# Performance work log

Hardware: AMD Instinct MI355X
Metric: run time of the kernel (lower is better)

Reference implementation:

```python
import jax, jax.numpy as jnp
import numpy as np

B, E, C = 512, 512, 100000
S, M, LAMDA, ALPHA = 30.0, 0.35, 0.01, 0.5  # s, m, lamda from init; ALPHA = args.alpha (center lr)
EPS = 1e-6


def setup_inputs() -> dict:
    key = jax.random.key(0)
    k1, k2, k3, k4 = jax.random.split(key, 4)
    embedding = jax.random.normal(k1, (B, E), dtype=jnp.float32)
    weights = jax.random.normal(k2, (C, E), dtype=jnp.float32)  # kaiming-init classifier weights
    centers = jax.random.normal(k3, (C, E), dtype=jnp.float32)  # class centers buffer
    label = jax.random.randint(k4, (B,), 0, C, dtype=jnp.int64)
    return {"embedding": embedding, "weights": weights, "centers": centers, "label": label}


def reference(embedding, weights, centers, label):
    rows = jnp.arange(B)
    # LMCL (CosFace) logits: cosine similarity via L2-normalized features and weights
    emb_n = embedding / jnp.linalg.norm(embedding, axis=1, keepdims=True)
    w_n = weights / jnp.linalg.norm(weights, axis=1, keepdims=True)
    logits = jnp.einsum('be,ce->bc', emb_n, w_n)            # [B, C]
    # subtract margin m at the target class, then scale by s
    m_logits = S * logits.at[rows, label].add(-M)
    logp = jax.nn.log_softmax(m_logits, axis=1)
    lmcl_loss = -jnp.mean(logp[rows, label])
    # top-1 precision (%)
    prec = jnp.mean((jnp.argmax(m_logits, axis=1) == label).astype(jnp.float32)) * 100.0
    # center loss: MSE between features and their class centers (centers treated as constant)
    centers_batch = centers[label]                           # [B, E] gather
    center_loss = jnp.mean((embedding - centers_batch) ** 2)
    # center update: scatter-subtract mean-normalized diff (replaces the python loop)
    counts = jnp.zeros((C,), dtype=jnp.float32).at[label].add(1.0)
    appear = counts[label]                                   # [B]
    diff = ALPHA * (centers_batch - embedding) / (appear[:, None] + EPS)
    new_centers = centers.at[label].add(-diff)
    total_loss = lmcl_loss + LAMDA * center_loss
    return prec, total_loss, new_centers
```

## Files before the change

### kernel.cpp

```cpp
#include <hip/hip_runtime.h>
#include <cstdint>
#include <cstddef>

#define B_ROWS 512
#define E_DIM  512
#define C_CLS  100000
#define NT     782

#define S_SC    30.0f
#define M_MRG   0.35f
#define LAMBDA_ 0.01f
#define ALPHA_  0.5f
#define EPS_    1e-6f

#define BM 128
#define BN 128
#define BK 64
#define LPAD 8

typedef __attribute__((ext_vector_type(8))) short bf16x8;
typedef __attribute__((ext_vector_type(4))) float f32x4;

static_assert((size_t)NT * BN >= C_CLS, "tile count");

constexpr size_t WS_PSUM  = 0;
constexpr size_t WS_PMAX  = WS_PSUM + (size_t)NT * B_ROWS * 4;
constexpr size_t WS_CLOSS = WS_PMAX + (size_t)NT * B_ROWS * 4;
constexpr size_t WS_EMBN  = WS_CLOSS + 512;
constexpr size_t WS_IEN   = WS_EMBN + (size_t)B_ROWS * E_DIM * 2;
constexpr size_t WS_COSL  = WS_IEN + 2048;
constexpr size_t WS_CNT   = WS_COSL + 2048;
constexpr size_t WS_RSUM  = WS_CNT + 2048;
constexpr size_t WS_RMAX  = WS_RSUM + 2048;
constexpr size_t WS_WBF   = 4 * 1024 * 1024;
constexpr size_t WS_NEED  = WS_WBF + (size_t)C_CLS * E_DIM * 2;

__device__ __forceinline__ unsigned short f2bf(float f) {
    unsigned u = __float_as_uint(f);
    u += 0x7fffu + ((u >> 16) & 1u);
    return (unsigned short)(u >> 16);
}
__device__ __forceinline__ unsigned fkey(float f) {
    unsigned u = __float_as_uint(f);
    return (u & 0x80000000u) ? ~u : (u | 0x80000000u);
}
__device__ __forceinline__ float unkey(unsigned k) {
    unsigned u = (k & 0x80000000u) ? (k ^ 0x80000000u) : ~k;
    return __uint_as_float(u);
}
__device__ __forceinline__ float waveReduceSum(float v) {
#pragma unroll
    for (int d = 1; d < 64; d <<= 1) v += __shfl_xor(v, d, 64);
    return v;
}
__device__ __forceinline__ unsigned waveReduceMax(unsigned v) {
#pragma unroll
    for (int d = 1; d < 64; d <<= 1) { unsigned o = __shfl_xor(v, d, 64); v = o > v ? o : v; }
    return v;
}
__device__ __forceinline__ float blockReduceSum256(float v, float* s4) {
    v = waveReduceSum(v);
    int w = threadIdx.x >> 6;
    if ((threadIdx.x & 63) == 0) s4[w] = v;
    __syncthreads();
    float r = s4[0] + s4[1] + s4[2] + s4[3];
    __syncthreads();
    return r;
}
__device__ __forceinline__ void g2l16(const void* g, void* l) {
    __builtin_amdgcn_global_load_lds(
        (const __attribute__((address_space(1))) unsigned int*)g,
        (__attribute__((address_space(3))) unsigned int*)l, 16, 0, 0);
}


__global__ __launch_bounds__(256) void emb_prep(const float* __restrict__ emb,
                                                unsigned short* __restrict__ embn,
                                                float* __restrict__ ien) {
    __shared__ float s4[4];
    int b = blockIdx.x, t = threadIdx.x;
    float2 v = *(const float2*)(emb + (size_t)b * E_DIM + t * 2);
    float ss = blockReduceSum256(v.x * v.x + v.y * v.y, s4);
    float inv = 1.0f / sqrtf(ss);
    ushort2 o; o.x = f2bf(v.x * inv); o.y = f2bf(v.y * inv);
    *(ushort2*)(embn + (size_t)b * E_DIM + t * 2) = o;
    if (t == 0) ien[b] = inv;
}

__global__ __launch_bounds__(256) void w_prep(const float* __restrict__ W,
                                              unsigned short* __restrict__ wbf) {
    int row = blockIdx.x * 4 + (threadIdx.x >> 6);
    int lane = threadIdx.x & 63;
    const float* src = W + (size_t)row * E_DIM;
    f32x4 a = *(const f32x4*)(src + lane * 4);
    f32x4 b = *(const f32x4*)(src + 256 + lane * 4);
    float ss = a.x*a.x + a.y*a.y + a.z*a.z + a.w*a.w
             + b.x*b.x + b.y*b.y + b.z*b.z + b.w*b.w;
    ss = waveReduceSum(ss);
    float inv = 1.0f / sqrtf(fmaxf(ss, 1e-30f));
    ushort4 o0, o1;
    o0.x = f2bf(a.x*inv); o0.y = f2bf(a.y*inv); o0.z = f2bf(a.z*inv); o0.w = f2bf(a.w*inv);
    o1.x = f2bf(b.x*inv); o1.y = f2bf(b.y*inv); o1.z = f2bf(b.z*inv); o1.w = f2bf(b.w*inv);
    *(ushort4*)(wbf + (size_t)row * E_DIM + lane * 4) = o0;
    *(ushort4*)(wbf + (size_t)row * E_DIM + 256 + lane * 4) = o1;
}

__global__ __launch_bounds__(256) void label_stats(const float* __restrict__ emb,
                                                   const float* __restrict__ W,
                                                   const float* __restrict__ centers,
                                                   const int* __restrict__ label,
                                                   const float* __restrict__ ien,
                                                   float* __restrict__ cosl,
                                                   float* __restrict__ cntf,
                                                   float* __restrict__ closs) {
    __shared__ float s4[4];
    int b = blockIdx.x, t = threadIdx.x;
    int lab = label[b];
    float d = 0.f, wss = 0.f, sq = 0.f;
    for (int c = t; c < E_DIM; c += 256) {
        float e  = emb[(size_t)b * E_DIM + c];
        float w  = W[(size_t)lab * E_DIM + c];
        float ce = centers[(size_t)lab * E_DIM + c];
        d += e * w; wss += w * w;
        float df = e - ce; sq += df * df;
    }
    float cn = ((label[t] == lab) ? 1.f : 0.f) + ((label[t + 256] == lab) ? 1.f : 0.f);
    d   = blockReduceSum256(d, s4);
    wss = blockReduceSum256(wss, s4);
    sq  = blockReduceSum256(sq, s4);
    cn  = blockReduceSum256(cn, s4);
    if (t == 0) {
        cosl[b] = d * ien[b] / sqrtf(wss);
        cntf[b] = cn;
        atomicAdd(closs, sq);
    }
}

__global__ __launch_bounds__(256) void gemm_fast(const unsigned short* __restrict__ embn,
                                                 const unsigned short* __restrict__ wbf,
                                                 const int* __restrict__ label,
                                                 float* __restrict__ psum,
                                                 unsigned* __restrict__ pmax) {
    __shared__ __align__(16) unsigned short sA[BM * BK];
    __shared__ __align__(16) unsigned short sB[BN * BK];
    __shared__ int      sLab[BM];
    __shared__ float    sSum[BM];
    __shared__ unsigned sMax[BM];

    const int tid = threadIdx.x;
    const int n0 = blockIdx.x * BN;
    const int lane = tid & 63, wave = tid >> 6;
    const int wm = wave >> 1, wn = wave & 1;
    const int q = lane >> 4, lm = lane & 15;
    const int lm7 = lm & 7;

    int aOff[4];
    const unsigned short* bP[4];
    unsigned short *aD[4], *bD[4];
#pragma unroll
    for (int j = 0; j < 4; ++j) {
        int G = j * 256 + tid;
        int r = G >> 3, p = G & 7, l = p ^ (r & 7);
        aOff[j] = r * E_DIM + l * 8;
        int rg = n0 + r; if (rg >= C_CLS) rg = 0;
        bP[j] = wbf + (size_t)rg * E_DIM + l * 8;
        aD[j] = &sA[(j * 256 + wave * 64) * 8];
        bD[j] = &sB[(j * 256 + wave * 64) * 8];
    }

    for (int m = 0; m < 4; ++m) {
        if (tid < BM) { sLab[tid] = label[m * BM + tid]; sSum[tid] = 0.f; sMax[tid] = 0u; }
        const unsigned short* aBase = embn + (size_t)m * BM * E_DIM;

        f32x4 acc[4][4];
#pragma unroll
        for (int i = 0; i < 4; ++i)
#pragma unroll
            for (int j = 0; j < 4; ++j) acc[i][j] = (f32x4){0.f, 0.f, 0.f, 0.f};

        for (int k0 = 0; k0 < E_DIM; k0 += BK) {
            __syncthreads();
#pragma unroll
            for (int j = 0; j < 4; ++j) g2l16(aBase + aOff[j] + k0, aD[j]);
#pragma unroll
            for (int j = 0; j < 4; ++j) g2l16(bP[j] + k0, bD[j]);
            __syncthreads();
#pragma unroll
            for (int kk = 0; kk < BK; kk += 32) {
                const int pg = ((kk >> 3) + q) ^ lm7;
                bf16x8 af[4], bfr[4];
#pragma unroll
                for (int i = 0; i < 4; ++i)
                    af[i] = *(const bf16x8*)&sA[(wm * 64 + i * 16 + lm) * BK + pg * 8];
#pragma unroll
                for (int j = 0; j < 4; ++j)
                    bfr[j] = *(const bf16x8*)&sB[(wn * 64 + j * 16 + lm) * BK + pg * 8];
#pragma unroll
                for (int i = 0; i < 4; ++i)
#pragma unroll
                    for (int j = 0; j < 4; ++j)
                        acc[i][j] = __builtin_amdgcn_mfma_f32_16x16x32_bf16(af[i], bfr[j], acc[i][j], 0, 0, 0);
            }
        }

#pragma unroll
        for (int i = 0; i < 4; ++i) {
#pragma unroll
            for (int r = 0; r < 4; ++r) {
                int row_l = wm * 64 + i * 16 + q * 4 + r;
                int lab = sLab[row_l];
                float sum = 0.f, mx = -1e30f;
#pragma unroll
                for (int j = 0; j < 4; ++j) {
                    int col_l = wn * 64 + j * 16 + lm;
                    int col = n0 + col_l;
                    float v = S_SC * acc[i][j][r];
                    if (col < C_CLS && col != lab) {
                        sum += __expf(v - 30.0f);
                        mx = fmaxf(mx, v);
                    }
                }
#pragma unroll
                for (int d = 1; d < 16; d <<= 1) {
                    sum += __shfl_xor(sum, d, 64);
                    mx = fmaxf(mx, __shfl_xor(mx, d, 64));
                }
                if (lm == 0) {
                    atomicAdd(&sSum[row_l], sum);
                    atomicMax(&sMax[row_l], fkey(mx));
                }
            }
        }
        __syncthreads();
        if (tid < BM) {
            psum[(size_t)blockIdx.x * B_ROWS + m * BM + tid] = sSum[tid];
            pmax[(size_t)blockIdx.x * B_ROWS + m * BM + tid] = sMax[tid];
        }
    }
}

__global__ __launch_bounds__(256) void gemm_slow(const unsigned short* __restrict__ embn,
                                                 const float* __restrict__ W,
                                                 const int* __restrict__ label,
                                                 float* __restrict__ psum,
                                                 unsigned* __restrict__ pmax) {
    __shared__ __align__(16) unsigned short sA[BM][BK + LPAD];
    __shared__ __align__(16) unsigned short sB[BN][BK + LPAD];
    __shared__ int      sLab[BM];
    __shared__ float    sSum[BM];
    __shared__ unsigned sMax[BM];
    __shared__ float    sInvN[BN];

    const int tid = threadIdx.x;
    const int m0 = blockIdx.x * BM;
    const int n0 = blockIdx.y * BN;
    if (tid < BM) { sLab[tid] = label[m0 + tid]; sSum[tid] = 0.f; sMax[tid] = 0u; }

    const int lane = tid & 63;
    const int wave = tid >> 6;
    const int wm = wave >> 1, wn = wave & 1;
    const int q = lane >> 4, lm = lane & 15;

    const int arow = tid >> 3, ac8 = tid & 7;
    const int brow = tid >> 4, bc4 = tid & 15;

    f32x4 acc[4][4];
#pragma unroll
    for (int i = 0; i < 4; ++i)
#pragma unroll
        for (int j = 0; j < 4; ++j) acc[i][j] = (f32x4){0.f, 0.f, 0.f, 0.f};

    float rss[8];
#pragma unroll
    for (int j = 0; j < 8; ++j) rss[j] = 0.f;

    const float* wb = W + (size_t)(n0 + brow) * E_DIM + bc4 * 4;

    for (int k0 = 0; k0 < E_DIM; k0 += BK) {
        __syncthreads();
#pragma unroll
        for (int j = 0; j < 4; ++j) {
            int rr = arow + 32 * j;
            uint4 v = *(const uint4*)(embn + (size_t)(m0 + rr) * E_DIM + k0 + ac8 * 8);
            *(uint4*)(&sA[rr][ac8 * 8]) = v;
        }
#pragma unroll
        for (int j = 0; j < 8; ++j) {
            int rr = brow + 16 * j;
            f32x4 v = (f32x4){0.f, 0.f, 0.f, 0.f};
            if (n0 + rr < C_CLS) v = *(const f32x4*)(wb + (size_t)(16 * j) * E_DIM + k0);
            rss[j] += v.x * v.x + v.y * v.y + v.z * v.z + v.w * v.w;
            ushort4 o; o.x = f2bf(v.x); o.y = f2bf(v.y); o.z = f2bf(v.z); o.w = f2bf(v.w);
            *(ushort4*)(&sB[rr][bc4 * 4]) = o;
        }
        __syncthreads();
#pragma unroll
        for (int kk = 0; kk < BK; kk += 32) {
            bf16x8 af[4], bfr[4];
#pragma unroll
            for (int i = 0; i < 4; ++i)
                af[i] = *(const bf16x8*)(&sA[wm * 64 + i * 16 + lm][kk + q * 8]);
#pragma unroll
            for (int j = 0; j < 4; ++j)
                bfr[j] = *(const bf16x8*)(&sB[wn * 64 + j * 16 + lm][kk + q * 8]);
#pragma unroll
            for (int i = 0; i < 4; ++i)
#pragma unroll
                for (int j = 0; j < 4; ++j)
                    acc[i][j] = __builtin_amdgcn_mfma_f32_16x16x32_bf16(af[i], bfr[j], acc[i][j], 0, 0, 0);
        }
    }
#pragma unroll
    for (int j = 0; j < 8; ++j) {
        float v = rss[j];
#pragma unroll
        for (int d = 1; d < 16; d <<= 1) v += __shfl_xor(v, d, 64);
        if (bc4 == 0) sInvN[brow + 16 * j] = rsqrtf(fmaxf(v, 1e-30f));
    }
    __syncthreads();
#pragma unroll
    for (int i = 0; i < 4; ++i) {
#pragma unroll
        for (int r = 0; r < 4; ++r) {
            int row_l = wm * 64 + i * 16 + q * 4 + r;
            int lab = sLab[row_l];
            float sum = 0.f, mx = -1e30f;
#pragma unroll
            for (int j = 0; j < 4; ++j) {
                int col_l = wn * 64 + j * 16 + lm;
                int col = n0 + col_l;
                float v = S_SC * acc[i][j][r] * sInvN[col_l];
                if (col < C_CLS && col != lab) {
                    sum += __expf(v - 30.0f);
                    mx = fmaxf(mx, v);
                }
            }
#pragma unroll
            for (int d = 1; d < 16; d <<= 1) {
                sum += __shfl_xor(sum, d, 64);
                mx = fmaxf(mx, __shfl_xor(mx, d, 64));
            }
            if (lm == 0) {
                atomicAdd(&sSum[row_l], sum);
                atomicMax(&sMax[row_l], fkey(mx));
            }
        }
    }
    __syncthreads();
    if (tid < BM) {
        psum[(size_t)blockIdx.y * B_ROWS + m0 + tid] = sSum[tid];
        pmax[(size_t)blockIdx.y * B_ROWS + m0 + tid] = sMax[tid];
    }
}

__global__ __launch_bounds__(256) void row_reduce(const float* __restrict__ psum,
                                                  const unsigned* __restrict__ pmax,
                                                  float* __restrict__ rsum,
                                                  float* __restrict__ rmax) {
    __shared__ float s4[4];
    __shared__ unsigned m4[4];
    int b = blockIdx.x, t = threadIdx.x;
    float s = 0.f; unsigned mk = 0u;
    for (int nt = t; nt < NT; nt += 256) {
        s += psum[(size_t)nt * B_ROWS + b];
        unsigned k = pmax[(size_t)nt * B_ROWS + b];
        mk = k > mk ? k : mk;
    }
    s = waveReduceSum(s);
    mk = waveReduceMax(mk);
    int w = t >> 6;
    if ((t & 63) == 0) { s4[w] = s; m4[w] = mk; }
    __syncthreads();
    if (t == 0) {
        rsum[b] = s4[0] + s4[1] + s4[2] + s4[3];
        unsigned m = m4[0];
#pragma unroll
        for (int i = 1; i < 4; ++i) m = m4[i] > m ? m4[i] : m;
        rmax[b] = unkey(m);
    }
}

__global__ __launch_bounds__(256) void finalize(const float* __restrict__ cosl,
                                                const float* __restrict__ rsum,
                                                const float* __restrict__ rmax,
                                                const float* __restrict__ closs,
                                                float* __restrict__ out) {
    __shared__ float s4[4];
    int t = threadIdx.x;
    float lsum = 0.f, msum = 0.f;
    for (int b = t; b < B_ROWS; b += 256) {
        float lv = S_SC * (cosl[b] - M_MRG);
        float tot = rsum[b] + __expf(lv - 30.0f);
        lsum += (logf(tot) + 30.0f) - lv;
        msum += (lv > rmax[b]) ? 1.0f : 0.0f;
    }
    lsum = blockReduceSum256(lsum, s4);
    msum = blockReduceSum256(msum, s4);
    if (t == 0) {
        out[0] = msum * (100.0f / (float)B_ROWS);
        out[1] = lsum * (1.0f / (float)B_ROWS)
               + LAMBDA_ * closs[0] * (1.0f / ((float)B_ROWS * (float)E_DIM));
    }
}

__global__ __launch_bounds__(256) void centers_copy(const float* __restrict__ src,
                                                    float* __restrict__ dst) {
    size_t i = (size_t)blockIdx.x * blockDim.x + threadIdx.x;
    size_t stride = (size_t)gridDim.x * blockDim.x;
    size_t n2 = (size_t)C_CLS * E_DIM / 2;
    const float2* s2 = (const float2*)src;
    float2* d2 = (float2*)dst;
    for (size_t k = i; k < n2; k += stride) d2[k] = s2[k];
}

__global__ __launch_bounds__(256) void scatter_upd(const float* __restrict__ emb,
                                                   const float* __restrict__ centers,
                                                   const int* __restrict__ label,
                                                   const float* __restrict__ cntf,
                                                   float* __restrict__ outC) {
    int b = blockIdx.x, t = threadIdx.x;
    int lab = label[b];
    float sc = ALPHA_ / (cntf[b] + EPS_);
    for (int c = t; c < E_DIM; c += 256) {
        float add = sc * (emb[(size_t)b * E_DIM + c] - centers[(size_t)lab * E_DIM + c]);
        atomicAdd(outC + (size_t)lab * E_DIM + c, add);
    }
}

extern "C" void kernel_launch(void* const* d_in, const int* in_sizes, int n_in,
                              void* d_out, int out_size, void* d_ws, size_t ws_size,
                              hipStream_t stream) {
    const float* emb     = (const float*)d_in[0];
    const float* W       = (const float*)d_in[1];
    const float* centers = (const float*)d_in[2];
    const int*   label   = (const int*)d_in[3];
    float* out = (float*)d_out;
    char* ws = (char*)d_ws;

    float*          psum = (float*)(ws + WS_PSUM);
    unsigned*       pmax = (unsigned*)(ws + WS_PMAX);
    float*          closs = (float*)(ws + WS_CLOSS);
    unsigned short* embn = (unsigned short*)(ws + WS_EMBN);
    float*          ien  = (float*)(ws + WS_IEN);
    float*          cosl = (float*)(ws + WS_COSL);
    float*          cntf = (float*)(ws + WS_CNT);
    float*          rsum = (float*)(ws + WS_RSUM);
    float*          rmax = (float*)(ws + WS_RMAX);
    unsigned short* wbf  = (unsigned short*)(ws + WS_WBF);

    hipMemsetAsync(ws + WS_CLOSS, 0, 512, stream);

    emb_prep<<<B_ROWS, 256, 0, stream>>>(emb, embn, ien);
    label_stats<<<B_ROWS, 256, 0, stream>>>(emb, W, centers, label, ien, cosl, cntf, closs);
    if (ws_size >= WS_NEED) {
        w_prep<<<C_CLS / 4, 256, 0, stream>>>(W, wbf);
        gemm_fast<<<NT, 256, 0, stream>>>(embn, wbf, label, psum, pmax);
    } else {
        gemm_slow<<<dim3(B_ROWS / BM, NT), 256, 0, stream>>>(embn, W, label, psum, pmax);
    }
    row_reduce<<<B_ROWS, 256, 0, stream>>>(psum, pmax, rsum, rmax);
    finalize<<<1, 256, 0, stream>>>(cosl, rsum, rmax, closs, out);
    centers_copy<<<12500, 256, 0, stream>>>(centers, out + 2);
    scatter_upd<<<B_ROWS, 256, 0, stream>>>(emb, centers, label, cntf, out + 2);
}
```

Measured before the change: 642.9 us.

## Restructure fast GEMM into 512-thread full-M tiles with triple-buffered async loads

The bf16 GEMM now uses 512-thread blocks that each cover all 512 embedding rows against a 128-class tile, instead of looping over four 128-row M chunks. It streams K in 32-wide steps through a three-slot LDS ring with a vmcnt-based wait, so global loads overlap the MFMA work and the W tile is read once per block. Row partials are written with global atomics into a workspace that is now zeroed by a larger memset. The centers copy is also changed to use aligned float4 stores. The cost is one block per CU with higher register pressure, plus the extra memset traffic.

```diff
diff --git a/kernel.cpp b/kernel.cpp
--- a/kernel.cpp
+++ b/kernel.cpp
@@ -18,10 +18,16 @@
 #define BK 64
 #define LPAD 8
 
+#define GBN    128
+#define GBK    32
+#define GSTEPS 16
+#define A_GRAN 2048
+#define SLOT_GRAN 2560
+
 typedef __attribute__((ext_vector_type(8))) short bf16x8;
 typedef __attribute__((ext_vector_type(4))) float f32x4;
 
-static_assert((size_t)NT * BN >= C_CLS, "tile count");
+static_assert((size_t)NT * GBN >= C_CLS, "tile count");
 
 constexpr size_t WS_PSUM  = 0;
 constexpr size_t WS_PMAX  = WS_PSUM + (size_t)NT * B_ROWS * 4;
@@ -136,105 +142,112 @@
     }
 }
 
-__global__ __launch_bounds__(256) void gemm_fast(const unsigned short* __restrict__ embn,
-                                                 const unsigned short* __restrict__ wbf,
-                                                 const int* __restrict__ label,
-                                                 float* __restrict__ psum,
-                                                 unsigned* __restrict__ pmax) {
-    __shared__ __align__(16) unsigned short sA[BM * BK];
-    __shared__ __align__(16) unsigned short sB[BN * BK];
-    __shared__ int      sLab[BM];
-    __shared__ float    sSum[BM];
-    __shared__ unsigned sMax[BM];
-
-    const int tid = threadIdx.x;
-    const int n0 = blockIdx.x * BN;
+__global__ __launch_bounds__(512, 1) void gemm_fast(const unsigned short* __restrict__ embn,
+                                                    const unsigned short* __restrict__ wbf,
+                                                    const int* __restrict__ label,
+                                                    float* __restrict__ psum,
+                                                    unsigned* __restrict__ pmax) {
+    __shared__ __align__(16) unsigned short sbuf[3][SLOT_GRAN * 8];
+    __shared__ int sLab[B_ROWS];
+
+    const int tid  = threadIdx.x;
     const int lane = tid & 63, wave = tid >> 6;
     const int wm = wave >> 1, wn = wave & 1;
     const int q = lane >> 4, lm = lane & 15;
-    const int lm7 = lm & 7;
-
+    const int n0 = blockIdx.x * GBN;
+
+    if (tid < B_ROWS) sLab[tid] = label[tid];
+
+    const int swz = (tid & 3) ^ ((tid >> 3) & 3);
     int aOff[4];
-    const unsigned short* bP[4];
-    unsigned short *aD[4], *bD[4];
 #pragma unroll
     for (int j = 0; j < 4; ++j) {
-        int G = j * 256 + tid;
-        int r = G >> 3, p = G & 7, l = p ^ (r & 7);
-        aOff[j] = r * E_DIM + l * 8;
-        int rg = n0 + r; if (rg >= C_CLS) rg = 0;
-        bP[j] = wbf + (size_t)rg * E_DIM + l * 8;
-        aD[j] = &sA[(j * 256 + wave * 64) * 8];
-        bD[j] = &sB[(j * 256 + wave * 64) * 8];
-    }
-
-    for (int m = 0; m < 4; ++m) {
-        if (tid < BM) { sLab[tid] = label[m * BM + tid]; sSum[tid] = 0.f; sMax[tid] = 0u; }
-        const unsigned short* aBase = embn + (size_t)m * BM * E_DIM;
-
-        f32x4 acc[4][4];
-#pragma unroll
-        for (int i = 0; i < 4; ++i)
-#pragma unroll
-            for (int j = 0; j < 4; ++j) acc[i][j] = (f32x4){0.f, 0.f, 0.f, 0.f};
-
-        for (int k0 = 0; k0 < E_DIM; k0 += BK) {
-            __syncthreads();
-#pragma unroll
-            for (int j = 0; j < 4; ++j) g2l16(aBase + aOff[j] + k0, aD[j]);
-#pragma unroll
-            for (int j = 0; j < 4; ++j) g2l16(bP[j] + k0, bD[j]);
-            __syncthreads();
-#pragma unroll
-            for (int kk = 0; kk < BK; kk += 32) {
-                const int pg = ((kk >> 3) + q) ^ lm7;
-                bf16x8 af[4], bfr[4];
-#pragma unroll
-                for (int i = 0; i < 4; ++i)
-                    af[i] = *(const bf16x8*)&sA[(wm * 64 + i * 16 + lm) * BK + pg * 8];
-#pragma unroll
-                for (int j = 0; j < 4; ++j)
-                    bfr[j] = *(const bf16x8*)&sB[(wn * 64 + j * 16 + lm) * BK + pg * 8];
-#pragma unroll
-                for (int i = 0; i < 4; ++i)
-#pragma unroll
-                    for (int j = 0; j < 4; ++j)
-                        acc[i][j] = __builtin_amdgcn_mfma_f32_16x16x32_bf16(af[i], bfr[j], acc[i][j], 0, 0, 0);
-            }
-        }
-
-#pragma unroll
-        for (int i = 0; i < 4; ++i) {
-#pragma unroll
-            for (int r = 0; r < 4; ++r) {
-                int row_l = wm * 64 + i * 16 + q * 4 + r;
-                int lab = sLab[row_l];
-                float sum = 0.f, mx = -1e30f;
-#pragma unroll
-                for (int j = 0; j < 4; ++j) {
-                    int col_l = wn * 64 + j * 16 + lm;
-                    int col = n0 + col_l;
-                    float v = S_SC * acc[i][j][r];
-                    if (col < C_CLS && col != lab) {
-                        sum += __expf(v - 30.0f);
-                        mx = fmaxf(mx, v);
-                    }
+        int r = j * 128 + (tid >> 2);
+        aOff[j] = r * (E_DIM * 2) + swz * 16;
+    }
+    int rb = n0 + (tid >> 2); if (rb >= C_CLS) rb = 0;
+    const size_t bOff = (size_t)rb * (E_DIM * 2) + (size_t)swz * 16;
+
+    const char* aBase = (const char*)embn;
+    const char* bBase = (const char*)wbf;
+
+    f32x4 acc[8][4];
+#pragma unroll
+    for (int i = 0; i < 8; ++i)
+#pragma unroll
+        for (int j = 0; j < 4; ++j) acc[i][j] = (f32x4){0.f, 0.f, 0.f, 0.f};
+
+#pragma unroll
+    for (int s = 0; s < 2; ++s) {
+        unsigned short* d = &sbuf[s][0];
+        const int kb = s * (GBK * 2);
+#pragma unroll
+        for (int j = 0; j < 4; ++j)
+            g2l16(aBase + aOff[j] + kb, d + (j * 512 + wave * 64) * 8);
+        g2l16(bBase + bOff + kb, d + (A_GRAN + wave * 64) * 8);
+    }
+
+    const int pq16 = (q ^ ((lm >> 1) & 3)) * 16;
+
+    int sc = 0, ss = 2;
+    for (int t = 0; t < GSTEPS; ++t) {
+        if (t < GSTEPS - 1)
+            asm volatile("s_waitcnt vmcnt(5) lgkmcnt(0)\n\ts_barrier" ::: "memory");
+        else
+            asm volatile("s_waitcnt vmcnt(0) lgkmcnt(0)\n\ts_barrier" ::: "memory");
+
+        const char* sb = (const char*)&sbuf[sc][0];
+        bf16x8 af[8], bfr[4];
+#pragma unroll
+        for (int i = 0; i < 8; ++i)
+            af[i] = *(const bf16x8*)(sb + (wm * 128 + i * 16 + lm) * 64 + pq16);
+#pragma unroll
+        for (int j = 0; j < 4; ++j)
+            bfr[j] = *(const bf16x8*)(sb + A_GRAN * 16 + (wn * 64 + j * 16 + lm) * 64 + pq16);
+#pragma unroll
+        for (int i = 0; i < 8; ++i)
+#pragma unroll
+            for (int j = 0; j < 4; ++j)
+                acc[i][j] = __builtin_amdgcn_mfma_f32_16x16x32_bf16(af[i], bfr[j], acc[i][j], 0, 0, 0);
+
+        if (t + 2 < GSTEPS) {
+            unsigned short* d = &sbuf[ss][0];
+            const int kb = (t + 2) * (GBK * 2);
+#pragma unroll
+            for (int j = 0; j < 4; ++j)
+                g2l16(aBase + aOff[j] + kb, d + (j * 512 + wave * 64) * 8);
+            g2l16(bBase + bOff + kb, d + (A_GRAN + wave * 64) * 8);
+        }
+        sc = (sc == 2) ? 0 : sc + 1;
+        ss = (ss == 2) ? 0 : ss + 1;
+    }
+
+    const size_t pbase = (size_t)blockIdx.x * B_ROWS;
+#pragma unroll
+    for (int i = 0; i < 8; ++i) {
+#pragma unroll
+        for (int r = 0; r < 4; ++r) {
+            int row = wm * 128 + i * 16 + q * 4 + r;
+            int lab = sLab[row];
+            float sum = 0.f, mx = -1e30f;
+#pragma unroll
+            for (int j = 0; j < 4; ++j) {
+                int col = n0 + wn * 64 + j * 16 + lm;
+                float v = S_SC * acc[i][j][r];
+                if (col < C_CLS && col != lab) {
+                    sum += __expf(v - 30.0f);
+                    mx = fmaxf(mx, v);
                 }
-#pragma unroll
-                for (int d = 1; d < 16; d <<= 1) {
-                    sum += __shfl_xor(sum, d, 64);
-                    mx = fmaxf(mx, __shfl_xor(mx, d, 64));
-                }
-                if (lm == 0) {
-                    atomicAdd(&sSum[row_l], sum);
-                    atomicMax(&sMax[row_l], fkey(mx));
-                }
-            }
-        }
-        __syncthreads();
-        if (tid < BM) {
-            psum[(size_t)blockIdx.x * B_ROWS + m * BM + tid] = sSum[tid];
-            pmax[(size_t)blockIdx.x * B_ROWS + m * BM + tid] = sMax[tid];
+            }
+#pragma unroll
+            for (int d = 1; d < 16; d <<= 1) {
+                sum += __shfl_xor(sum, d, 64);
+                mx = fmaxf(mx, __shfl_xor(mx, d, 64));
+            }
+            if (lm == 0) {
+                atomicAdd(&psum[pbase + row], sum);
+                atomicMax(&pmax[pbase + row], fkey(mx));
+            }
         }
     }
 }
@@ -407,10 +420,19 @@
                                                     float* __restrict__ dst) {
     size_t i = (size_t)blockIdx.x * blockDim.x + threadIdx.x;
     size_t stride = (size_t)gridDim.x * blockDim.x;
-    size_t n2 = (size_t)C_CLS * E_DIM / 2;
-    const float2* s2 = (const float2*)src;
-    float2* d2 = (float2*)dst;
-    for (size_t k = i; k < n2; k += stride) d2[k] = s2[k];
+    constexpr size_t N  = (size_t)C_CLS * E_DIM;
+    constexpr size_t n4 = (N - 2) / 4;
+    const float2* s2 = (const float2*)(src + 2);
+    float4* d4 = (float4*)(dst + 2);
+    for (size_t k = i; k < n4; k += stride) {
+        float2 a = s2[2 * k], b = s2[2 * k + 1];
+        d4[k] = make_float4(a.x, a.y, b.x, b.y);
+    }
+    if (i == 0) {
+        *(float2*)dst = *(const float2*)src;
+        constexpr size_t t0 = 2 + 4 * n4;
+        *(float2*)(dst + t0) = *(const float2*)(src + t0);
+    }
 }
 
 __global__ __launch_bounds__(256) void scatter_upd(const float* __restrict__ emb,
@@ -448,13 +470,13 @@
     float*          rmax = (float*)(ws + WS_RMAX);
     unsigned short* wbf  = (unsigned short*)(ws + WS_WBF);
 
-    hipMemsetAsync(ws + WS_CLOSS, 0, 512, stream);
+    hipMemsetAsync(ws, 0, WS_CLOSS + 512, stream);
 
     emb_prep<<<B_ROWS, 256, 0, stream>>>(emb, embn, ien);
     label_stats<<<B_ROWS, 256, 0, stream>>>(emb, W, centers, label, ien, cosl, cntf, closs);
     if (ws_size >= WS_NEED) {
         w_prep<<<C_CLS / 4, 256, 0, stream>>>(W, wbf);
-        gemm_fast<<<NT, 256, 0, stream>>>(embn, wbf, label, psum, pmax);
+        gemm_fast<<<NT, 512, 0, stream>>>(embn, wbf, label, psum, pmax);
     } else {
         gemm_slow<<<dim3(B_ROWS / BM, NT), 256, 0, stream>>>(embn, W, label, psum, pmax);
     }
```

New measurement: 602.5 us. 6.3% less time.
